# Kernel tuning notes

Measured on AMD Instinct MI355X. Metric: run time of the kernel, lower is better.

Reference implementation:

```python
import jax, jax.numpy as jnp
import numpy as np

N, E = 100_000, 1_600_000
C_IN = C_OUT = 2


def _ln(h, g, b, eps=1e-5):
    mu = h.mean(-1, keepdims=True)
    var = ((h - mu) ** 2).mean(-1, keepdims=True)
    return (h - mu) * jax.lax.rsqrt(var + eps) * g + b


def _radial(x, W1, b1, g1, be1, W2, b2, g2, be2, W3, b3):
    h = jax.nn.relu(_ln(x @ W1 + b1, g1, be1))
    h = jax.nn.relu(_ln(h @ W2 + b2, g2, be2))
    return h @ W3 + b3


def setup_inputs() -> dict:
    key = jax.random.key(0)
    ks = jax.random.split(key, 20)
    inp = {
        "f0": jax.random.normal(ks[0], (N, C_IN, 1), jnp.float32),
        "f1": jax.random.normal(ks[1], (N, C_IN, 3), jnp.float32),
        "dist": jax.random.uniform(ks[2], (E,), jnp.float32),
        "u": jax.random.randint(ks[3], (E,), 0, N),
        "v": jax.random.randint(ks[4], (E,), 0, N),
        "wq": 0.5 * jax.random.normal(ks[5], (2, C_OUT, C_IN), jnp.float32),
        "wj00": jax.random.normal(ks[6], (E, 1, 1, 1), jnp.float32),
        "wj01": jax.random.normal(ks[7], (E, 1, 1, 3), jnp.float32),
        "wj10": jax.random.normal(ks[8], (E, 1, 3, 1), jnp.float32),
        "wj11": jax.random.normal(ks[9], (E, 3, 3, 3), jnp.float32),
        # radial MLP params for the 4 WLayers, index i = 2*l + k
        "rW1": 0.5 * jax.random.normal(ks[10], (4, C_IN + 1, 16), jnp.float32),
        "rb1": jnp.zeros((4, 16), jnp.float32),
        "g1": jnp.ones((4, 16), jnp.float32),
        "be1": jnp.zeros((4, 16), jnp.float32),
        "rW2": 0.3 * jax.random.normal(ks[11], (4, 16, 16), jnp.float32),
        "rb2": jnp.zeros((4, 16), jnp.float32),
        "g2": jnp.ones((4, 16), jnp.float32),
        "be2": jnp.zeros((4, 16), jnp.float32),
        "W3_00": 0.3 * jax.random.normal(ks[12], (16, 4), jnp.float32),
        "b3_00": jnp.zeros((4,), jnp.float32),
        "W3_01": 0.3 * jax.random.normal(ks[13], (16, 4), jnp.float32),
        "b3_01": jnp.zeros((4,), jnp.float32),
        "W3_10": 0.3 * jax.random.normal(ks[14], (16, 4), jnp.float32),
        "b3_10": jnp.zeros((4,), jnp.float32),
        "W3_11": 0.3 * jax.random.normal(ks[15], (16, 12), jnp.float32),
        "b3_11": jnp.zeros((12,), jnp.float32),
    }
    return inp


def reference(f0, f1, dist, u, v, wq, wj00, wj01, wj10, wj11,
              rW1, rb1, g1, be1, rW2, rb2, g2, be2,
              W3_00, b3_00, W3_01, b3_01, W3_10, b3_10, W3_11, b3_11):
    n = f0.shape[0]
    e = u.shape[0]
    # calc_q: [N, c_out, sum(2k+1)=4]
    q = jnp.concatenate([jnp.einsum('oi,nik->nok', wq[0], f0),
                         jnp.einsum('oi,nik->nok', wq[1], f1)], axis=2)
    # per-edge radial input: [dot(f0_src, f0_dst) over rep dim, dist] -> [E, c_in+1]
    vec = jnp.concatenate([jnp.sum(f0[u] * f0[v], axis=2), dist[:, None]], axis=1)
    f_dst = (f0[v], f1[v])  # edges.dst[k]
    wjs = {(0, 0): wj00, (0, 1): wj01, (1, 0): wj10, (1, 1): wj11}
    W3s = {(0, 0): (W3_00, b3_00), (0, 1): (W3_01, b3_01),
           (1, 0): (W3_10, b3_10), (1, 1): (W3_11, b3_11)}
    # calc_k: for each output degree l, sum over input degrees k of
    #   einsum('ejoi,ejlk,eik->eol', R, w_j, f_dst[k])  (fused form of the
    #   original 'ejoi,ejlk->eoilk' then 'eoilk,eik->eol')
    kl = []
    for l in range(2):
        acc = jnp.zeros((e, C_OUT, 2 * l + 1), f0.dtype)
        for k in range(2):
            i = 2 * l + k
            W3, b3 = W3s[(l, k)]
            J = 2 * min(k, l) + 1
            R = _radial(vec, rW1[i], rb1[i], g1[i], be1[i],
                        rW2[i], rb2[i], g2[i], be2[i], W3, b3)
            R = R.reshape(e, J, C_OUT, C_IN)
            acc = acc + jnp.einsum('ejoi,ejlk,eik->eol', R, wjs[(l, k)], f_dst[k])
        kl.append(acc)
    k_feat = jnp.concatenate(kl, axis=2)  # [E, c_out, 4]
    dot = jnp.einsum('eol,eol->e', q[v], k_feat)  # [E]
    # scatter logsumexp over destination nodes, then edge softmax weights
    m = jax.lax.stop_gradient(jax.ops.segment_max(dot, v, num_segments=n))
    m = jnp.where(jnp.isfinite(m), m, 0.0)
    ssum = jax.ops.segment_sum(jnp.exp(dot - m[v]), v, num_segments=n)
    lse = m + jnp.log(ssum)
    return jnp.exp(dot - lse[v])
```

## Files before the change

kernel.cpp:

```cpp
#include <hip/hip_runtime.h>
#include <math.h>


#define TPB 256

typedef float f2 __attribute__((ext_vector_type(2)));
typedef int i2 __attribute__((ext_vector_type(2)));

static __device__ __forceinline__ f2 fma2(f2 a, f2 b, f2 c) {
    return __builtin_elementwise_fma(a, b, c);
}
static __device__ __forceinline__ f2 splat(float x) {
    f2 r;
    r.x = x;
    r.y = x;
    return r;
}
static __device__ __forceinline__ float get16(const f2* h, int c) {
    return (c & 1) ? h[c >> 1].y : h[c >> 1].x;
}

static __device__ __forceinline__ double exp_wide(float d) {
    d = fminf(fmaxf(d, -1400.f), 1400.f);
    const float t = d * 1.44269504088896340736f;
    const float k = rintf(t);
    const float p = exp2f(t - k);
    const int ik = (int)k;
    const int k1 = ik >> 1;
    const int k2 = ik - k1;
    const double s1 = __hiloint2double((k1 + 1023) << 20, 0);
    const double s2 = __hiloint2double((k2 + 1023) << 20, 0);
    return ((double)p * s1) * s2;
}

static __device__ __forceinline__ void ln_relu16(f2* h, const float* __restrict__ g,
                                                 const float* __restrict__ be) {
    const f2* g2 = (const f2*)g;
    const f2* be2 = (const f2*)be;
    f2 s = h[0] + h[1] + h[2] + h[3] + h[4] + h[5] + h[6] + h[7];
    const float mu = (s.x + s.y) * 0.0625f;
    const f2 mu2 = splat(mu);
    f2 vs = splat(0.f);
#pragma unroll
    for (int i = 0; i < 8; ++i) {
        f2 d = h[i] - mu2;
        vs = fma2(d, d, vs);
    }
    const float var = (vs.x + vs.y) * 0.0625f;
    const f2 r2 = splat(rsqrtf(var + 1e-5f));
    const f2 zero = splat(0.f);
#pragma unroll
    for (int i = 0; i < 8; ++i) {
        f2 t = (h[i] - mu2) * r2;
        h[i] = __builtin_elementwise_max(fma2(t, g2[i], be2[i]), zero);
    }
}

__global__ __launch_bounds__(TPB, 4) void edge_kernel(
    const float* __restrict__ f0, const float* __restrict__ f1,
    const float* __restrict__ dist, const int* __restrict__ u,
    const int* __restrict__ v, const float* __restrict__ wq,
    const float* __restrict__ wj00, const float* __restrict__ wj01,
    const float* __restrict__ wj10, const float* __restrict__ wj11,
    const float* __restrict__ rW1, const float* __restrict__ rb1,
    const float* __restrict__ g1, const float* __restrict__ be1,
    const float* __restrict__ rW2, const float* __restrict__ rb2,
    const float* __restrict__ g2, const float* __restrict__ be2,
    const float* __restrict__ W3_00, const float* __restrict__ b3_00,
    const float* __restrict__ W3_01, const float* __restrict__ b3_01,
    const float* __restrict__ W3_10, const float* __restrict__ b3_10,
    const float* __restrict__ W3_11, const float* __restrict__ b3_11,
    float* __restrict__ out, double* __restrict__ ssum, int E) {
    const int e = blockIdx.x * blockDim.x + threadIdx.x;
    if (e >= E) return;

    const int uu = __builtin_nontemporal_load(u + e);
    const int vv = v[e];

    const float f0u0 = f0[uu * 2 + 0];
    const float f0u1 = f0[uu * 2 + 1];
    const float f0v0 = f0[vv * 2 + 0];
    const float f0v1 = f0[vv * 2 + 1];
    float f1v[2][3];
#pragma unroll
    for (int i = 0; i < 2; ++i)
#pragma unroll
        for (int m = 0; m < 3; ++m) f1v[i][m] = f1[vv * 6 + i * 3 + m];

    const float vec0 = f0u0 * f0v0;
    const float vec1 = f0u1 * f0v1;
    const float vec2 = __builtin_nontemporal_load(dist + e);

    float acc0[2] = {0.f, 0.f};
    float acc1[2][3] = {{0.f, 0.f, 0.f}, {0.f, 0.f, 0.f}};

#pragma clang loop unroll(disable)
    for (int i = 0; i < 4; ++i) {
        const float* W1 = rW1 + i * 48;
        const float* b1 = rb1 + i * 16;
        const float* g1i = g1 + i * 16;
        const float* be1i = be1 + i * 16;
        const float* W2 = rW2 + i * 256;
        const float* b2 = rb2 + i * 16;
        const float* g2i = g2 + i * 16;
        const float* be2i = be2 + i * 16;

        f2 h[8];
        {
            const f2* W1r0 = (const f2*)W1;
            const f2* W1r1 = (const f2*)(W1 + 16);
            const f2* W1r2 = (const f2*)(W1 + 32);
            const f2* b1v = (const f2*)b1;
            const f2 a = splat(vec0), b = splat(vec1), c = splat(vec2);
#pragma unroll
            for (int j = 0; j < 8; ++j)
                h[j] = fma2(a, W1r0[j],
                            fma2(b, W1r1[j], fma2(c, W1r2[j], b1v[j])));
        }
        ln_relu16(h, g1i, be1i);

        f2 h2[8];
        {
            const f2* b2v = (const f2*)b2;
#pragma unroll
            for (int j = 0; j < 8; ++j) h2[j] = b2v[j];
#pragma unroll
            for (int c = 0; c < 16; ++c) {
                const f2 hc = splat(get16(h, c));
                const f2* row = (const f2*)(W2 + c * 16);
#pragma unroll
                for (int j = 0; j < 8; ++j) h2[j] = fma2(hc, row[j], h2[j]);
            }
        }
        ln_relu16(h2, g2i, be2i);

        if (i == 3) {
#pragma unroll
            for (int j = 0; j < 3; ++j) {
                f2 p0 = *(const f2*)(b3_11 + j * 4);
                f2 p1 = *(const f2*)(b3_11 + j * 4 + 2);
#pragma unroll
                for (int c = 0; c < 16; ++c) {
                    const f2 hc = splat(get16(h2, c));
                    p0 = fma2(hc, *(const f2*)(W3_11 + c * 12 + j * 4), p0);
                    p1 = fma2(hc, *(const f2*)(W3_11 + c * 12 + j * 4 + 2), p1);
                }
#pragma unroll
                for (int m = 0; m < 3; ++m) {
                    const float w0 = __builtin_nontemporal_load(
                        wj11 + e * 27 + j * 9 + m * 3 + 0);
                    const float w1 = __builtin_nontemporal_load(
                        wj11 + e * 27 + j * 9 + m * 3 + 1);
                    const float w2 = __builtin_nontemporal_load(
                        wj11 + e * 27 + j * 9 + m * 3 + 2);
                    const float B0 =
                        w0 * f1v[0][0] + w1 * f1v[0][1] + w2 * f1v[0][2];
                    const float B1 =
                        w0 * f1v[1][0] + w1 * f1v[1][1] + w2 * f1v[1][2];
                    acc1[0][m] += p0.x * B0 + p0.y * B1;
                    acc1[1][m] += p1.x * B0 + p1.y * B1;
                }
            }
        } else {
            const float* W3p;
            const float* b3p;
            if (i == 0) {
                W3p = W3_00;
                b3p = b3_00;
            } else if (i == 1) {
                W3p = W3_01;
                b3p = b3_01;
            } else {
                W3p = W3_10;
                b3p = b3_10;
            }
            f2 p0 = *(const f2*)(b3p);
            f2 p1 = *(const f2*)(b3p + 2);
#pragma unroll
            for (int c = 0; c < 16; ++c) {
                const f2 hc = splat(get16(h2, c));
                p0 = fma2(hc, *(const f2*)(W3p + c * 4), p0);
                p1 = fma2(hc, *(const f2*)(W3p + c * 4 + 2), p1);
            }
            if (i == 0) {
                const float w = __builtin_nontemporal_load(wj00 + e);
                acc0[0] += w * (p0.x * f0v0 + p0.y * f0v1);
                acc0[1] += w * (p1.x * f0v0 + p1.y * f0v1);
            } else if (i == 1) {
                const float w0 = __builtin_nontemporal_load(wj01 + e * 3 + 0);
                const float w1 = __builtin_nontemporal_load(wj01 + e * 3 + 1);
                const float w2 = __builtin_nontemporal_load(wj01 + e * 3 + 2);
                const float s0 =
                    w0 * f1v[0][0] + w1 * f1v[0][1] + w2 * f1v[0][2];
                const float s1 =
                    w0 * f1v[1][0] + w1 * f1v[1][1] + w2 * f1v[1][2];
                acc0[0] += p0.x * s0 + p0.y * s1;
                acc0[1] += p1.x * s0 + p1.y * s1;
            } else {
                const float t0 = p0.x * f0v0 + p0.y * f0v1;
                const float t1 = p1.x * f0v0 + p1.y * f0v1;
#pragma unroll
                for (int m = 0; m < 3; ++m) {
                    const float w =
                        __builtin_nontemporal_load(wj10 + e * 3 + m);
                    acc1[0][m] += w * t0;
                    acc1[1][m] += w * t1;
                }
            }
        }
    }

    float dot = 0.f;
    {
        const float q00 = wq[0] * f0v0 + wq[1] * f0v1;
        const float q01 = wq[2] * f0v0 + wq[3] * f0v1;
        dot += q00 * acc0[0] + q01 * acc0[1];
#pragma unroll
        for (int m = 0; m < 3; ++m) {
            const float q1m0 = wq[4] * f1v[0][m] + wq[5] * f1v[1][m];
            const float q1m1 = wq[6] * f1v[0][m] + wq[7] * f1v[1][m];
            dot += q1m0 * acc1[0][m] + q1m1 * acc1[1][m];
        }
    }

    __builtin_nontemporal_store(dot, out + e);
    atomicAdd(&ssum[vv], exp_wide(dot));
}

__global__ void norm_kernel(float* __restrict__ out, const int* __restrict__ v,
                            const double* __restrict__ ssum, int E) {
    const int t = blockIdx.x * blockDim.x + threadIdx.x;
    const int e0 = t * 2;
    if (e0 >= E) return;
    if (e0 + 1 < E) {
        const f2 dv = *((const f2*)out + t);
        const i2 vv = *((const i2*)v + t);
        const double s0 = ssum[vv.x];
        const double s1 = ssum[vv.y];
        f2 r;
        r.x = (float)(exp_wide(dv.x) / s0);
        r.y = (float)(exp_wide(dv.y) / s1);
        __builtin_nontemporal_store(r, (f2*)out + t);
    } else {
        out[e0] = (float)(exp_wide(out[e0]) / ssum[v[e0]]);
    }
}

extern "C" void kernel_launch(void* const* d_in, const int* in_sizes, int n_in,
                              void* d_out, int out_size, void* d_ws,
                              size_t ws_size, hipStream_t stream) {
    const float* f0 = (const float*)d_in[0];
    const float* f1 = (const float*)d_in[1];
    const float* dist = (const float*)d_in[2];
    const int* u = (const int*)d_in[3];
    const int* v = (const int*)d_in[4];
    const float* wq = (const float*)d_in[5];
    const float* wj00 = (const float*)d_in[6];
    const float* wj01 = (const float*)d_in[7];
    const float* wj10 = (const float*)d_in[8];
    const float* wj11 = (const float*)d_in[9];
    const float* rW1 = (const float*)d_in[10];
    const float* rb1 = (const float*)d_in[11];
    const float* g1 = (const float*)d_in[12];
    const float* be1 = (const float*)d_in[13];
    const float* rW2 = (const float*)d_in[14];
    const float* rb2 = (const float*)d_in[15];
    const float* g2 = (const float*)d_in[16];
    const float* be2 = (const float*)d_in[17];
    const float* W3_00 = (const float*)d_in[18];
    const float* b3_00 = (const float*)d_in[19];
    const float* W3_01 = (const float*)d_in[20];
    const float* b3_01 = (const float*)d_in[21];
    const float* W3_10 = (const float*)d_in[22];
    const float* b3_10 = (const float*)d_in[23];
    const float* W3_11 = (const float*)d_in[24];
    const float* b3_11 = (const float*)d_in[25];

    const int N = in_sizes[0] / 2;
    const int E = in_sizes[2];

    double* ssum = (double*)d_ws;
    float* out = (float*)d_out;

    const int ge = (E + TPB - 1) / TPB;
    const int gp = ((E + 1) / 2 + TPB - 1) / TPB;

    hipMemsetAsync(ssum, 0, (size_t)N * sizeof(double), stream);
    edge_kernel<<<ge, TPB, 0, stream>>>(
        f0, f1, dist, u, v, wq, wj00, wj01, wj10, wj11, rW1, rb1, g1, be1, rW2,
        rb2, g2, be2, W3_00, b3_00, W3_01, b3_01, W3_10, b3_10, W3_11, b3_11,
        out, ssum, E);
    norm_kernel<<<gp, TPB, 0, stream>>>(out, v, ssum, E);
}
```

Measured before the change: 450.5 us.

## Stage MLP weights in LDS and prefetch all per-edge wj loads upfront

Copies all radial MLP weights, biases and wq into a shared-memory block at kernel start, so the inner loop reads them from LDS instead of through scalar/global loads. It also hoists every per-edge streaming load (dist, wj00, wj01, wj10, wj11) to the top of the kernel so their latency overlaps the MLP compute. The cost is about 8KB of LDS per block, a block-wide sync, and roughly 34 extra live registers, which may reduce occupancy under the 4-waves launch bound. Uniform weights were previously likely served by scalar loads, so moving them to LDS could add per-lane LDS traffic.

```diff
diff --git a/kernel.cpp b/kernel.cpp
--- a/kernel.cpp
+++ b/kernel.cpp
@@ -33,8 +33,8 @@
     return ((double)p * s1) * s2;
 }
 
-static __device__ __forceinline__ void ln_relu16(f2* h, const float* __restrict__ g,
-                                                 const float* __restrict__ be) {
+static __device__ __forceinline__ void ln_relu16(f2* h, const float* g,
+                                                 const float* be) {
     const f2* g2 = (const f2*)g;
     const f2* be2 = (const f2*)be;
     f2 s = h[0] + h[1] + h[2] + h[3] + h[4] + h[5] + h[6] + h[7];
@@ -55,6 +55,8 @@
         h[i] = __builtin_elementwise_max(fma2(t, g2[i], be2[i]), zero);
     }
 }
+
+#define LDSW 2016
 
 __global__ __launch_bounds__(TPB, 4) void edge_kernel(
     const float* __restrict__ f0, const float* __restrict__ f1,
@@ -71,11 +73,49 @@
     const float* __restrict__ W3_10, const float* __restrict__ b3_10,
     const float* __restrict__ W3_11, const float* __restrict__ b3_11,
     float* __restrict__ out, double* __restrict__ ssum, int E) {
+    __shared__ float W[LDSW];
+    {
+        const int t = threadIdx.x;
+        for (int i = t; i < 192; i += TPB) W[0 + i] = rW1[i];
+        if (t < 64) W[192 + t] = rb1[t];
+        if (t < 64) W[256 + t] = g1[t];
+        if (t < 64) W[320 + t] = be1[t];
+        for (int i = t; i < 1024; i += TPB) W[384 + i] = rW2[i];
+        if (t < 64) W[1408 + t] = rb2[t];
+        if (t < 64) W[1472 + t] = g2[t];
+        if (t < 64) W[1536 + t] = be2[t];
+        if (t < 64) W[1600 + t] = W3_00[t];
+        if (t < 4) W[1664 + t] = b3_00[t];
+        if (t < 64) W[1668 + t] = W3_01[t];
+        if (t < 4) W[1732 + t] = b3_01[t];
+        if (t < 64) W[1736 + t] = W3_10[t];
+        if (t < 4) W[1800 + t] = b3_10[t];
+        for (int i = t; i < 192; i += TPB) W[1804 + i] = W3_11[i];
+        if (t < 12) W[1996 + t] = b3_11[t];
+        if (t < 8) W[2008 + t] = wq[t];
+    }
+    __syncthreads();
+
     const int e = blockIdx.x * blockDim.x + threadIdx.x;
     if (e >= E) return;
 
     const int uu = __builtin_nontemporal_load(u + e);
     const int vv = v[e];
+    const float dd = __builtin_nontemporal_load(dist + e);
+    const float w00 = __builtin_nontemporal_load(wj00 + e);
+    float w01[3], w10[3], w11[27];
+    {
+        const float* p01 = wj01 + (size_t)e * 3;
+        const float* p10 = wj10 + (size_t)e * 3;
+        const float* p11 = wj11 + (size_t)e * 27;
+#pragma unroll
+        for (int c = 0; c < 3; ++c) w01[c] = __builtin_nontemporal_load(p01 + c);
+#pragma unroll
+        for (int c = 0; c < 3; ++c) w10[c] = __builtin_nontemporal_load(p10 + c);
+#pragma unroll
+        for (int c = 0; c < 27; ++c)
+            w11[c] = __builtin_nontemporal_load(p11 + c);
+    }
 
     const float f0u0 = f0[uu * 2 + 0];
     const float f0u1 = f0[uu * 2 + 1];
@@ -89,21 +129,21 @@
 
     const float vec0 = f0u0 * f0v0;
     const float vec1 = f0u1 * f0v1;
-    const float vec2 = __builtin_nontemporal_load(dist + e);
+    const float vec2 = dd;
 
     float acc0[2] = {0.f, 0.f};
     float acc1[2][3] = {{0.f, 0.f, 0.f}, {0.f, 0.f, 0.f}};
 
 #pragma clang loop unroll(disable)
     for (int i = 0; i < 4; ++i) {
-        const float* W1 = rW1 + i * 48;
-        const float* b1 = rb1 + i * 16;
-        const float* g1i = g1 + i * 16;
-        const float* be1i = be1 + i * 16;
-        const float* W2 = rW2 + i * 256;
-        const float* b2 = rb2 + i * 16;
-        const float* g2i = g2 + i * 16;
-        const float* be2i = be2 + i * 16;
+        const float* W1 = W + i * 48;
+        const float* b1 = W + 192 + i * 16;
+        const float* g1i = W + 256 + i * 16;
+        const float* be1i = W + 320 + i * 16;
+        const float* W2 = W + 384 + i * 256;
+        const float* b2 = W + 1408 + i * 16;
+        const float* g2i = W + 1472 + i * 16;
+        const float* be2i = W + 1536 + i * 16;
 
         f2 h[8];
         {
@@ -135,45 +175,34 @@
         ln_relu16(h2, g2i, be2i);
 
         if (i == 3) {
+            const float* W3p = W + 1804;
+            const float* b3p = W + 1996;
 #pragma unroll
             for (int j = 0; j < 3; ++j) {
-                f2 p0 = *(const f2*)(b3_11 + j * 4);
-                f2 p1 = *(const f2*)(b3_11 + j * 4 + 2);
+                f2 p0 = *(const f2*)(b3p + j * 4);
+                f2 p1 = *(const f2*)(b3p + j * 4 + 2);
 #pragma unroll
                 for (int c = 0; c < 16; ++c) {
                     const f2 hc = splat(get16(h2, c));
-                    p0 = fma2(hc, *(const f2*)(W3_11 + c * 12 + j * 4), p0);
-                    p1 = fma2(hc, *(const f2*)(W3_11 + c * 12 + j * 4 + 2), p1);
+                    p0 = fma2(hc, *(const f2*)(W3p + c * 12 + j * 4), p0);
+                    p1 = fma2(hc, *(const f2*)(W3p + c * 12 + j * 4 + 2), p1);
                 }
 #pragma unroll
                 for (int m = 0; m < 3; ++m) {
-                    const float w0 = __builtin_nontemporal_load(
-                        wj11 + e * 27 + j * 9 + m * 3 + 0);
-                    const float w1 = __builtin_nontemporal_load(
-                        wj11 + e * 27 + j * 9 + m * 3 + 1);
-                    const float w2 = __builtin_nontemporal_load(
-                        wj11 + e * 27 + j * 9 + m * 3 + 2);
+                    const float a0 = w11[j * 9 + m * 3 + 0];
+                    const float a1 = w11[j * 9 + m * 3 + 1];
+                    const float a2 = w11[j * 9 + m * 3 + 2];
                     const float B0 =
-                        w0 * f1v[0][0] + w1 * f1v[0][1] + w2 * f1v[0][2];
+                        a0 * f1v[0][0] + a1 * f1v[0][1] + a2 * f1v[0][2];
                     const float B1 =
-                        w0 * f1v[1][0] + w1 * f1v[1][1] + w2 * f1v[1][2];
+                        a0 * f1v[1][0] + a1 * f1v[1][1] + a2 * f1v[1][2];
                     acc1[0][m] += p0.x * B0 + p0.y * B1;
                     acc1[1][m] += p1.x * B0 + p1.y * B1;
                 }
             }
         } else {
-            const float* W3p;
-            const float* b3p;
-            if (i == 0) {
-                W3p = W3_00;
-                b3p = b3_00;
-            } else if (i == 1) {
-                W3p = W3_01;
-                b3p = b3_01;
-            } else {
-                W3p = W3_10;
-                b3p = b3_10;
-            }
+            const float* W3p = W + 1600 + i * 68;
+            const float* b3p = W3p + 64;
             f2 p0 = *(const f2*)(b3p);
             f2 p1 = *(const f2*)(b3p + 2);
 #pragma unroll
@@ -183,17 +212,13 @@
                 p1 = fma2(hc, *(const f2*)(W3p + c * 4 + 2), p1);
             }
             if (i == 0) {
-                const float w = __builtin_nontemporal_load(wj00 + e);
-                acc0[0] += w * (p0.x * f0v0 + p0.y * f0v1);
-                acc0[1] += w * (p1.x * f0v0 + p1.y * f0v1);
+                acc0[0] += w00 * (p0.x * f0v0 + p0.y * f0v1);
+                acc0[1] += w00 * (p1.x * f0v0 + p1.y * f0v1);
             } else if (i == 1) {
-                const float w0 = __builtin_nontemporal_load(wj01 + e * 3 + 0);
-                const float w1 = __builtin_nontemporal_load(wj01 + e * 3 + 1);
-                const float w2 = __builtin_nontemporal_load(wj01 + e * 3 + 2);
                 const float s0 =
-                    w0 * f1v[0][0] + w1 * f1v[0][1] + w2 * f1v[0][2];
+                    w01[0] * f1v[0][0] + w01[1] * f1v[0][1] + w01[2] * f1v[0][2];
                 const float s1 =
-                    w0 * f1v[1][0] + w1 * f1v[1][1] + w2 * f1v[1][2];
+                    w01[0] * f1v[1][0] + w01[1] * f1v[1][1] + w01[2] * f1v[1][2];
                 acc0[0] += p0.x * s0 + p0.y * s1;
                 acc0[1] += p1.x * s0 + p1.y * s1;
             } else {
@@ -201,10 +226,8 @@
                 const float t1 = p1.x * f0v0 + p1.y * f0v1;
 #pragma unroll
                 for (int m = 0; m < 3; ++m) {
-                    const float w =
-                        __builtin_nontemporal_load(wj10 + e * 3 + m);
-                    acc1[0][m] += w * t0;
-                    acc1[1][m] += w * t1;
+                    acc1[0][m] += w10[m] * t0;
+                    acc1[1][m] += w10[m] * t1;
                 }
             }
         }
@@ -212,13 +235,14 @@
 
     float dot = 0.f;
     {
-        const float q00 = wq[0] * f0v0 + wq[1] * f0v1;
-        const float q01 = wq[2] * f0v0 + wq[3] * f0v1;
+        const float* wqs = W + 2008;
+        const float q00 = wqs[0] * f0v0 + wqs[1] * f0v1;
+        const float q01 = wqs[2] * f0v0 + wqs[3] * f0v1;
         dot += q00 * acc0[0] + q01 * acc0[1];
 #pragma unroll
         for (int m = 0; m < 3; ++m) {
-            const float q1m0 = wq[4] * f1v[0][m] + wq[5] * f1v[1][m];
-            const float q1m1 = wq[6] * f1v[0][m] + wq[7] * f1v[1][m];
+            const float q1m0 = wqs[4] * f1v[0][m] + wqs[5] * f1v[1][m];
+            const float q1m1 = wqs[6] * f1v[0][m] + wqs[7] * f1v[1][m];
             dot += q1m0 * acc1[0][m] + q1m1 * acc1[1][m];
         }
     }
```

After: 987.9 us. +119.3%, slower.

## Process two edges per thread with packed f2 math across edges

Applied to the files above, without the earlier changes.

Each thread now handles two consecutive edges, and the float2 lanes hold the two edges instead of two MLP channels. All MLP, layernorm and contraction arithmetic runs as packed FMAs over the edge pair, with per-edge weights broadcast as scalars. Index, dist and wj00 loads become vector loads, but the nontemporal load hints on the per-edge wj arrays are dropped. The edge grid is halved and launch bounds are relaxed from 4 to 3 blocks per SM to leave room for the doubled register footprint, at some cost to occupancy.

```diff
diff --git a/kernel.cpp b/kernel.cpp
--- a/kernel.cpp
+++ b/kernel.cpp
@@ -16,8 +16,11 @@
     r.y = x;
     return r;
 }
-static __device__ __forceinline__ float get16(const f2* h, int c) {
-    return (c & 1) ? h[c >> 1].y : h[c >> 1].x;
+static __device__ __forceinline__ f2 mk2(float a, float b) {
+    f2 r;
+    r.x = a;
+    r.y = b;
+    return r;
 }
 
 static __device__ __forceinline__ double exp_wide(float d) {
@@ -33,30 +36,30 @@
     return ((double)p * s1) * s2;
 }
 
-static __device__ __forceinline__ void ln_relu16(f2* h, const float* __restrict__ g,
-                                                 const float* __restrict__ be) {
-    const f2* g2 = (const f2*)g;
-    const f2* be2 = (const f2*)be;
-    f2 s = h[0] + h[1] + h[2] + h[3] + h[4] + h[5] + h[6] + h[7];
-    const float mu = (s.x + s.y) * 0.0625f;
-    const f2 mu2 = splat(mu);
+static __device__ __forceinline__ void ln_relu16p(f2* h, const float* __restrict__ g,
+                                                  const float* __restrict__ be) {
+    f2 s = splat(0.f);
+#pragma unroll
+    for (int j = 0; j < 16; ++j) s = s + h[j];
+    const f2 mu = s * splat(0.0625f);
     f2 vs = splat(0.f);
 #pragma unroll
-    for (int i = 0; i < 8; ++i) {
-        f2 d = h[i] - mu2;
-        vs = fma2(d, d, vs);
-    }
-    const float var = (vs.x + vs.y) * 0.0625f;
-    const f2 r2 = splat(rsqrtf(var + 1e-5f));
+    for (int j = 0; j < 16; ++j) {
+        h[j] = h[j] - mu;
+        vs = fma2(h[j], h[j], vs);
+    }
+    const f2 var = vs * splat(0.0625f);
+    const f2 r = mk2(rsqrtf(var.x + 1e-5f), rsqrtf(var.y + 1e-5f));
     const f2 zero = splat(0.f);
 #pragma unroll
-    for (int i = 0; i < 8; ++i) {
-        f2 t = (h[i] - mu2) * r2;
-        h[i] = __builtin_elementwise_max(fma2(t, g2[i], be2[i]), zero);
-    }
-}
-
-__global__ __launch_bounds__(TPB, 4) void edge_kernel(
+    for (int j = 0; j < 16; ++j) {
+        const f2 t = h[j] * r;
+        h[j] = __builtin_elementwise_max(fma2(t, splat(g[j]), splat(be[j])),
+                                         zero);
+    }
+}
+
+__global__ __launch_bounds__(TPB, 3) void edge_kernel(
     const float* __restrict__ f0, const float* __restrict__ f1,
     const float* __restrict__ dist, const int* __restrict__ u,
     const int* __restrict__ v, const float* __restrict__ wq,
@@ -71,28 +74,60 @@
     const float* __restrict__ W3_10, const float* __restrict__ b3_10,
     const float* __restrict__ W3_11, const float* __restrict__ b3_11,
     float* __restrict__ out, double* __restrict__ ssum, int E) {
-    const int e = blockIdx.x * blockDim.x + threadIdx.x;
-    if (e >= E) return;
-
-    const int uu = __builtin_nontemporal_load(u + e);
-    const int vv = v[e];
-
-    const float f0u0 = f0[uu * 2 + 0];
-    const float f0u1 = f0[uu * 2 + 1];
-    const float f0v0 = f0[vv * 2 + 0];
-    const float f0v1 = f0[vv * 2 + 1];
-    float f1v[2][3];
-#pragma unroll
-    for (int i = 0; i < 2; ++i)
-#pragma unroll
-        for (int m = 0; m < 3; ++m) f1v[i][m] = f1[vv * 6 + i * 3 + m];
-
-    const float vec0 = f0u0 * f0v0;
-    const float vec1 = f0u1 * f0v1;
-    const float vec2 = __builtin_nontemporal_load(dist + e);
-
-    float acc0[2] = {0.f, 0.f};
-    float acc1[2][3] = {{0.f, 0.f, 0.f}, {0.f, 0.f, 0.f}};
+    const int t = blockIdx.x * blockDim.x + threadIdx.x;
+    const int e0 = t * 2;
+    if (e0 >= E) return;
+    const bool has1 = (e0 + 1) < E;
+    const int e1 = has1 ? e0 + 1 : e0;
+
+    int u0, u1, v0, v1;
+    f2 dd, w00;
+    if (has1) {
+        const i2 uu2 = *((const i2*)u + t);
+        const i2 vv2 = *((const i2*)v + t);
+        u0 = uu2.x;
+        u1 = uu2.y;
+        v0 = vv2.x;
+        v1 = vv2.y;
+        dd = *((const f2*)dist + t);
+        w00 = *((const f2*)wj00 + t);
+    } else {
+        u0 = u1 = u[e0];
+        v0 = v1 = v[e0];
+        dd = splat(dist[e0]);
+        w00 = splat(wj00[e0]);
+    }
+
+    const f2 a0 = *(const f2*)(f0 + (size_t)u0 * 2);
+    const f2 a1 = *(const f2*)(f0 + (size_t)u1 * 2);
+    const f2 b0 = *(const f2*)(f0 + (size_t)v0 * 2);
+    const f2 b1v_ = *(const f2*)(f0 + (size_t)v1 * 2);
+    const f2 fu0 = mk2(a0.x, a1.x);
+    const f2 fu1 = mk2(a0.y, a1.y);
+    const f2 fv0 = mk2(b0.x, b1v_.x);
+    const f2 fv1 = mk2(b0.y, b1v_.y);
+
+    f2 f1v[2][3];
+    {
+        const float* p0 = f1 + (size_t)v0 * 6;
+        const float* p1 = f1 + (size_t)v1 * 6;
+#pragma unroll
+        for (int i = 0; i < 2; ++i)
+#pragma unroll
+            for (int m = 0; m < 3; ++m)
+                f1v[i][m] = mk2(p0[i * 3 + m], p1[i * 3 + m]);
+    }
+
+    const f2 vec0 = fu0 * fv0;
+    const f2 vec1 = fu1 * fv1;
+    const f2 vec2 = dd;
+
+    f2 acc0[2] = {splat(0.f), splat(0.f)};
+    f2 acc1[2][3];
+#pragma unroll
+    for (int o = 0; o < 2; ++o)
+#pragma unroll
+        for (int m = 0; m < 3; ++m) acc1[o][m] = splat(0.f);
 
 #pragma clang loop unroll(disable)
     for (int i = 0; i < 4; ++i) {
@@ -105,60 +140,52 @@
         const float* g2i = g2 + i * 16;
         const float* be2i = be2 + i * 16;
 
-        f2 h[8];
-        {
-            const f2* W1r0 = (const f2*)W1;
-            const f2* W1r1 = (const f2*)(W1 + 16);
-            const f2* W1r2 = (const f2*)(W1 + 32);
-            const f2* b1v = (const f2*)b1;
-            const f2 a = splat(vec0), b = splat(vec1), c = splat(vec2);
-#pragma unroll
-            for (int j = 0; j < 8; ++j)
-                h[j] = fma2(a, W1r0[j],
-                            fma2(b, W1r1[j], fma2(c, W1r2[j], b1v[j])));
+        f2 h[16];
+#pragma unroll
+        for (int j = 0; j < 16; ++j)
+            h[j] = fma2(vec0, splat(W1[j]),
+                        fma2(vec1, splat(W1[16 + j]),
+                             fma2(vec2, splat(W1[32 + j]), splat(b1[j]))));
+        ln_relu16p(h, g1i, be1i);
+
+        f2 h2[16];
+#pragma unroll
+        for (int j = 0; j < 16; ++j) h2[j] = splat(b2[j]);
+#pragma unroll
+        for (int c = 0; c < 16; ++c) {
+#pragma unroll
+            for (int j = 0; j < 16; ++j)
+                h2[j] = fma2(h[c], splat(W2[c * 16 + j]), h2[j]);
         }
-        ln_relu16(h, g1i, be1i);
-
-        f2 h2[8];
-        {
-            const f2* b2v = (const f2*)b2;
-#pragma unroll
-            for (int j = 0; j < 8; ++j) h2[j] = b2v[j];
-#pragma unroll
-            for (int c = 0; c < 16; ++c) {
-                const f2 hc = splat(get16(h, c));
-                const f2* row = (const f2*)(W2 + c * 16);
-#pragma unroll
-                for (int j = 0; j < 8; ++j) h2[j] = fma2(hc, row[j], h2[j]);
-            }
-        }
-        ln_relu16(h2, g2i, be2i);
+        ln_relu16p(h2, g2i, be2i);
 
         if (i == 3) {
 #pragma unroll
             for (int j = 0; j < 3; ++j) {
-                f2 p0 = *(const f2*)(b3_11 + j * 4);
-                f2 p1 = *(const f2*)(b3_11 + j * 4 + 2);
+                f2 p00 = splat(b3_11[j * 4 + 0]);
+                f2 p01 = splat(b3_11[j * 4 + 1]);
+                f2 p10 = splat(b3_11[j * 4 + 2]);
+                f2 p11 = splat(b3_11[j * 4 + 3]);
 #pragma unroll
                 for (int c = 0; c < 16; ++c) {
-                    const f2 hc = splat(get16(h2, c));
-                    p0 = fma2(hc, *(const f2*)(W3_11 + c * 12 + j * 4), p0);
-                    p1 = fma2(hc, *(const f2*)(W3_11 + c * 12 + j * 4 + 2), p1);
+                    const f2 hc = h2[c];
+                    p00 = fma2(hc, splat(W3_11[c * 12 + j * 4 + 0]), p00);
+                    p01 = fma2(hc, splat(W3_11[c * 12 + j * 4 + 1]), p01);
+                    p10 = fma2(hc, splat(W3_11[c * 12 + j * 4 + 2]), p10);
+                    p11 = fma2(hc, splat(W3_11[c * 12 + j * 4 + 3]), p11);
                 }
 #pragma unroll
                 for (int m = 0; m < 3; ++m) {
-                    const float w0 = __builtin_nontemporal_load(
-                        wj11 + e * 27 + j * 9 + m * 3 + 0);
-                    const float w1 = __builtin_nontemporal_load(
-                        wj11 + e * 27 + j * 9 + m * 3 + 1);
-                    const float w2 = __builtin_nontemporal_load(
-                        wj11 + e * 27 + j * 9 + m * 3 + 2);
-                    const float B0 =
-                        w0 * f1v[0][0] + w1 * f1v[0][1] + w2 * f1v[0][2];
-                    const float B1 =
-                        w0 * f1v[1][0] + w1 * f1v[1][1] + w2 * f1v[1][2];
-                    acc1[0][m] += p0.x * B0 + p0.y * B1;
-                    acc1[1][m] += p1.x * B0 + p1.y * B1;
+                    const f2 c0 = mk2(wj11[(size_t)e0 * 27 + j * 9 + m * 3 + 0],
+                                      wj11[(size_t)e1 * 27 + j * 9 + m * 3 + 0]);
+                    const f2 c1 = mk2(wj11[(size_t)e0 * 27 + j * 9 + m * 3 + 1],
+                                      wj11[(size_t)e1 * 27 + j * 9 + m * 3 + 1]);
+                    const f2 c2 = mk2(wj11[(size_t)e0 * 27 + j * 9 + m * 3 + 2],
+                                      wj11[(size_t)e1 * 27 + j * 9 + m * 3 + 2]);
+                    const f2 B0 = c0 * f1v[0][0] + c1 * f1v[0][1] + c2 * f1v[0][2];
+                    const f2 B1 = c0 * f1v[1][0] + c1 * f1v[1][1] + c2 * f1v[1][2];
+                    acc1[0][m] = fma2(p00, B0, fma2(p01, B1, acc1[0][m]));
+                    acc1[1][m] = fma2(p10, B0, fma2(p11, B1, acc1[1][m]));
                 }
             }
         } else {
@@ -174,57 +201,66 @@
                 W3p = W3_10;
                 b3p = b3_10;
             }
-            f2 p0 = *(const f2*)(b3p);
-            f2 p1 = *(const f2*)(b3p + 2);
+            f2 p00 = splat(b3p[0]);
+            f2 p01 = splat(b3p[1]);
+            f2 p10 = splat(b3p[2]);
+            f2 p11 = splat(b3p[3]);
 #pragma unroll
             for (int c = 0; c < 16; ++c) {
-                const f2 hc = splat(get16(h2, c));
-                p0 = fma2(hc, *(const f2*)(W3p + c * 4), p0);
-                p1 = fma2(hc, *(const f2*)(W3p + c * 4 + 2), p1);
+                const f2 hc = h2[c];
+                p00 = fma2(hc, splat(W3p[c * 4 + 0]), p00);
+                p01 = fma2(hc, splat(W3p[c * 4 + 1]), p01);
+                p10 = fma2(hc, splat(W3p[c * 4 + 2]), p10);
+                p11 = fma2(hc, splat(W3p[c * 4 + 3]), p11);
             }
             if (i == 0) {
-                const float w = __builtin_nontemporal_load(wj00 + e);
-                acc0[0] += w * (p0.x * f0v0 + p0.y * f0v1);
-                acc0[1] += w * (p1.x * f0v0 + p1.y * f0v1);
+                acc0[0] = fma2(w00, fma2(p00, fv0, p01 * fv1), acc0[0]);
+                acc0[1] = fma2(w00, fma2(p10, fv0, p11 * fv1), acc0[1]);
             } else if (i == 1) {
-                const float w0 = __builtin_nontemporal_load(wj01 + e * 3 + 0);
-                const float w1 = __builtin_nontemporal_load(wj01 + e * 3 + 1);
-                const float w2 = __builtin_nontemporal_load(wj01 + e * 3 + 2);
-                const float s0 =
-                    w0 * f1v[0][0] + w1 * f1v[0][1] + w2 * f1v[0][2];
-                const float s1 =
-                    w0 * f1v[1][0] + w1 * f1v[1][1] + w2 * f1v[1][2];
-                acc0[0] += p0.x * s0 + p0.y * s1;
-                acc0[1] += p1.x * s0 + p1.y * s1;
+                f2 c0 = mk2(wj01[(size_t)e0 * 3 + 0], wj01[(size_t)e1 * 3 + 0]);
+                f2 c1 = mk2(wj01[(size_t)e0 * 3 + 1], wj01[(size_t)e1 * 3 + 1]);
+                f2 c2 = mk2(wj01[(size_t)e0 * 3 + 2], wj01[(size_t)e1 * 3 + 2]);
+                const f2 s0 = c0 * f1v[0][0] + c1 * f1v[0][1] + c2 * f1v[0][2];
+                const f2 s1 = c0 * f1v[1][0] + c1 * f1v[1][1] + c2 * f1v[1][2];
+                acc0[0] = fma2(p00, s0, fma2(p01, s1, acc0[0]));
+                acc0[1] = fma2(p10, s0, fma2(p11, s1, acc0[1]));
             } else {
-                const float t0 = p0.x * f0v0 + p0.y * f0v1;
-                const float t1 = p1.x * f0v0 + p1.y * f0v1;
+                const f2 t0 = fma2(p00, fv0, p01 * fv1);
+                const f2 t1 = fma2(p10, fv0, p11 * fv1);
 #pragma unroll
                 for (int m = 0; m < 3; ++m) {
-                    const float w =
-                        __builtin_nontemporal_load(wj10 + e * 3 + m);
-                    acc1[0][m] += w * t0;
-                    acc1[1][m] += w * t1;
+                    const f2 wm =
+                        mk2(wj10[(size_t)e0 * 3 + m], wj10[(size_t)e1 * 3 + m]);
+                    acc1[0][m] = fma2(wm, t0, acc1[0][m]);
+                    acc1[1][m] = fma2(wm, t1, acc1[1][m]);
                 }
             }
         }
     }
 
-    float dot = 0.f;
+    f2 dot = splat(0.f);
     {
-        const float q00 = wq[0] * f0v0 + wq[1] * f0v1;
-        const float q01 = wq[2] * f0v0 + wq[3] * f0v1;
-        dot += q00 * acc0[0] + q01 * acc0[1];
+        const f2 q00 = fma2(splat(wq[0]), fv0, splat(wq[1]) * fv1);
+        const f2 q01 = fma2(splat(wq[2]), fv0, splat(wq[3]) * fv1);
+        dot = fma2(q00, acc0[0], fma2(q01, acc0[1], dot));
 #pragma unroll
         for (int m = 0; m < 3; ++m) {
-            const float q1m0 = wq[4] * f1v[0][m] + wq[5] * f1v[1][m];
-            const float q1m1 = wq[6] * f1v[0][m] + wq[7] * f1v[1][m];
-            dot += q1m0 * acc1[0][m] + q1m1 * acc1[1][m];
+            const f2 q1m0 =
+                fma2(splat(wq[4]), f1v[0][m], splat(wq[5]) * f1v[1][m]);
+            const f2 q1m1 =
+                fma2(splat(wq[6]), f1v[0][m], splat(wq[7]) * f1v[1][m]);
+            dot = fma2(q1m0, acc1[0][m], fma2(q1m1, acc1[1][m], dot));
         }
     }
 
-    __builtin_nontemporal_store(dot, out + e);
-    atomicAdd(&ssum[vv], exp_wide(dot));
+    if (has1) {
+        __builtin_nontemporal_store(dot, (f2*)out + t);
+        atomicAdd(&ssum[v0], exp_wide(dot.x));
+        atomicAdd(&ssum[v1], exp_wide(dot.y));
+    } else {
+        out[e0] = dot.x;
+        atomicAdd(&ssum[v0], exp_wide(dot.x));
+    }
 }
 
 __global__ void norm_kernel(float* __restrict__ out, const int* __restrict__ v,
@@ -282,11 +318,10 @@
     double* ssum = (double*)d_ws;
     float* out = (float*)d_out;
 
-    const int ge = (E + TPB - 1) / TPB;
     const int gp = ((E + 1) / 2 + TPB - 1) / TPB;
 
     hipMemsetAsync(ssum, 0, (size_t)N * sizeof(double), stream);
-    edge_kernel<<<ge, TPB, 0, stream>>>(
+    edge_kernel<<<gp, TPB, 0, stream>>>(
         f0, f1, dist, u, v, wq, wj00, wj01, wj10, wj11, rW1, rb1, g1, be1, rW2,
         rb2, g2, be2, W3_00, b3_00, W3_01, b3_01, W3_10, b3_10, W3_11, b3_11,
         out, ssum, E);
```

Result: faster. 431.9 us (-4.1%).
